# Optimization experiments

Measured on AMD Instinct MI355X. Metric: run time of the kernel, lower is better.

Reference implementation:

```python
import jax, jax.numpy as jnp
import numpy as np

N, E, D = 100000, 1600000, 128

def setup_inputs() -> dict:
    key = jax.random.key(0)
    ks = jax.random.split(key, 6)
    x = jax.random.normal(ks[0], (N, D), dtype=jnp.float32)
    edge_index = jax.random.randint(ks[1], (2, E), 0, N, dtype=jnp.int64)
    edge_weight = jax.random.uniform(ks[2], (E, 1), dtype=jnp.float32)
    s = 1.0 / np.sqrt(D)  # glorot-ish scale
    W1 = jax.random.normal(ks[3], (D, D), dtype=jnp.float32) * s
    b1 = jnp.zeros((D,), dtype=jnp.float32)
    W2 = jax.random.normal(ks[4], (D, D), dtype=jnp.float32) * s
    b2 = jnp.zeros((D,), dtype=jnp.float32)
    return {"x": x, "edge_index": edge_index, "edge_weight": edge_weight,
            "W1": W1, "b1": b1, "W2": W2, "b2": b2}

def reference(x, edge_index, edge_weight, W1, b1, W2, b2):
    # wh_1 = w1(x)  -- computed in the original forward but unused (dead code)
    wh_1 = x @ W1 + b1
    # gather source-node features: [E, D]
    x_j = x[edge_index[0]]
    # edge_weight reshaped to [E, 1], elementwise scale
    ew = edge_weight.reshape(-1, 1)
    # scatter-sum into destination nodes: [N, D]
    agg = jax.ops.segment_sum(x_j * ew, edge_index[1], num_segments=x.shape[0])
    wh_2 = agg @ W2 + b2
    return wh_2
```

## Files before the change

### kernel.cpp

```cpp
#include <hip/hip_runtime.h>

#define D 128
#define BSH 9
#define BNODES 512
#define NBUK 256
#define CAP_B 9216
#define CAP_S 11264
#define EPB 8192

typedef __attribute__((ext_vector_type(4))) float f32x4;
typedef __attribute__((ext_vector_type(8))) short bf16x8;

__device__ __forceinline__ unsigned short f2bf(float f) {
    unsigned u = __float_as_uint(f);
    u += 0x7FFFu + ((u >> 16) & 1u);
    return (unsigned short)(u >> 16);
}
__device__ __forceinline__ unsigned pack2(float a, float b) {
    return (unsigned)f2bf(a) | ((unsigned)f2bf(b) << 16);
}
__device__ __forceinline__ float bflo(unsigned v) { return __uint_as_float(v << 16); }
__device__ __forceinline__ float bfhi(unsigned v) { return __uint_as_float(v & 0xFFFF0000u); }

__global__ __launch_bounds__(256) void cvt_x_kernel(
        const float4* __restrict__ x4, uint2* __restrict__ xb, int n4,
        const float* __restrict__ W2, unsigned short* __restrict__ w2b,
        int* __restrict__ bcur) {
    int tid = blockIdx.x * blockDim.x + threadIdx.x;
    int stride = gridDim.x * blockDim.x;
    for (int i = tid; i < n4; i += stride) {
        float4 v = x4[i];
        xb[i] = make_uint2(pack2(v.x, v.y), pack2(v.z, v.w));
    }
    if (tid < D * D) {
        int j = tid >> 7, k = tid & 127;
        w2b[tid] = f2bf(W2[k * D + j]);
    }
    if (tid < NBUK) bcur[tid] = 0;
}

__global__ __launch_bounds__(256) void binify_kernel(
        const int* __restrict__ ei, const float* __restrict__ ew,
        int* __restrict__ bcur, uint2* __restrict__ brec, int E) {
    __shared__ int lh[NBUK];
    __shared__ int lbase[NBUK];
    int t = threadIdx.x;
    int base0 = blockIdx.x * EPB;
    lh[t] = 0;
    __syncthreads();

    #pragma unroll 4
    for (int u = 0; u < EPB / 512; ++u) {
        int e = base0 + u * 512 + t * 2;
        if (e + 1 < E) {
            int2 d2 = *(const int2*)(ei + E + e);
            atomicAdd(&lh[d2.x >> BSH], 1);
            atomicAdd(&lh[d2.y >> BSH], 1);
        } else if (e < E) {
            atomicAdd(&lh[ei[E + e] >> BSH], 1);
        }
    }
    __syncthreads();
    lbase[t] = (lh[t] > 0) ? atomicAdd(&bcur[t], lh[t]) : 0;
    lh[t] = 0;
    __syncthreads();

    #pragma unroll 4
    for (int u = 0; u < EPB / 512; ++u) {
        int e = base0 + u * 512 + t * 2;
        if (e + 1 < E) {
            int2 s2 = *(const int2*)(ei + e);
            int2 d2 = *(const int2*)(ei + E + e);
            float2 w2 = *(const float2*)(ew + e);
            int b0 = d2.x >> BSH;
            int p0 = lbase[b0] + atomicAdd(&lh[b0], 1);
            if (p0 < CAP_B)
                brec[(size_t)b0 * CAP_B + p0] = make_uint2(
                    ((unsigned)s2.x << BSH) | (unsigned)(d2.x & (BNODES - 1)),
                    __float_as_uint(w2.x));
            int b1 = d2.y >> BSH;
            int p1 = lbase[b1] + atomicAdd(&lh[b1], 1);
            if (p1 < CAP_B)
                brec[(size_t)b1 * CAP_B + p1] = make_uint2(
                    ((unsigned)s2.y << BSH) | (unsigned)(d2.y & (BNODES - 1)),
                    __float_as_uint(w2.y));
        } else if (e < E) {
            int b0 = ei[E + e] >> BSH;
            int p0 = lbase[b0] + atomicAdd(&lh[b0], 1);
            if (p0 < CAP_B)
                brec[(size_t)b0 * CAP_B + p0] = make_uint2(
                    ((unsigned)ei[e] << BSH) | (unsigned)(ei[E + e] & (BNODES - 1)),
                    __float_as_uint(ew[e]));
        }
    }
}

__global__ __launch_bounds__(256) void nodeify_kernel(
        const uint2* __restrict__ brec, const int* __restrict__ bcur,
        unsigned* __restrict__ srec, int2* __restrict__ offcnt, int N) {
    __shared__ int nh[BNODES];
    __shared__ int nb[BNODES];
    int b = blockIdx.x;
    int t = threadIdx.x;
    int cnt = bcur[b];
    if (cnt > CAP_B) cnt = CAP_B;
    const uint2* rec = brec + (size_t)b * CAP_B;

    nh[t] = 0; nh[t + 256] = 0;
    __syncthreads();
    for (int i = t; i < cnt; i += 256)
        atomicAdd(&nh[rec[i].x & (BNODES - 1)], 1);
    __syncthreads();

    int c0 = nh[2 * t], c1 = nh[2 * t + 1];
    int c0p = (c0 + 7) & ~7, c1p = (c1 + 7) & ~7;
    int run = c0p + c1p;
    nb[t] = run;
    __syncthreads();
    int val = run;
    for (int off = 1; off < 256; off <<= 1) {
        int other = (t >= off) ? nb[t - off] : 0;
        __syncthreads();
        val += other;
        nb[t] = val;
        __syncthreads();
    }
    int excl = val - run;
    __syncthreads();
    nb[2 * t] = excl;
    nb[2 * t + 1] = excl + c0p;

    int sbase = b * CAP_S;
    int node0 = b * BNODES;
    if (node0 + 2 * t < N)     offcnt[node0 + 2 * t]     = make_int2(sbase + excl,       c0p);
    if (node0 + 2 * t + 1 < N) offcnt[node0 + 2 * t + 1] = make_int2(sbase + excl + c0p, c1p);
    for (int p = c0; p < c0p; ++p) srec[(size_t)sbase + excl + p] = 0u;
    for (int p = c1; p < c1p; ++p) srec[(size_t)sbase + excl + c0p + p] = 0u;

    __syncthreads();
    nh[t] = 0; nh[t + 256] = 0;
    __syncthreads();

    for (int i = t; i < cnt; i += 256) {
        uint2 r = rec[i];
        int nl = r.x & (BNODES - 1);
        int rk = atomicAdd(&nh[nl], 1);
        unsigned src = r.x >> BSH;
        float w = __uint_as_float(r.y);
        int w15 = __float2int_rn(w * 32768.f);
        w15 = w15 < 0 ? 0 : (w15 > 32767 ? 32767 : w15);
        srec[(size_t)sbase + nb[nl] + rk] = (src << 15) | (unsigned)w15;
    }
}

__global__ __launch_bounds__(1024, 8) void gg_kernel(
        const unsigned* __restrict__ xb,
        const unsigned* __restrict__ srec,
        const int2* __restrict__ offcnt,
        const unsigned short* __restrict__ w2b,
        const float* __restrict__ b2,
        float* __restrict__ out, int N) {
    __shared__ unsigned At[16 * 66];
    int t = threadIdx.x, wave = t >> 6, lane = t & 63;
    int node0 = blockIdx.x * 16;
    int node = node0 + wave;

    int2 oc = offcnt[node];
    int beg = oc.x, total = oc.y;
    const char* xbase = (const char*)xb + lane * 4;
    float ax = 0.f, ay = 0.f;

    if (total <= 64) {
        unsigned rec = srec[beg + (lane < total ? lane : 0)];
        for (int r = 0; r + 8 <= total; r += 8) {
            unsigned q[8], v[8];
            #pragma unroll
            for (int u = 0; u < 8; ++u) q[u] = __shfl(rec, r + u);
            #pragma unroll
            for (int u = 0; u < 8; ++u)
                v[u] = *(const unsigned*)(xbase + ((q[u] & 0xFFFF8000u) >> 7));
            #pragma unroll
            for (int u = 0; u < 8; ++u) {
                float w = (float)(q[u] & 32767u);
                ax = fmaf(bflo(v[u]), w, ax);
                ay = fmaf(bfhi(v[u]), w, ay);
            }
        }
    } else {
        for (int j = beg; j < beg + total; ++j) {
            unsigned q0 = srec[j];
            unsigned v0 = *(const unsigned*)(xbase + ((q0 & 0xFFFF8000u) >> 7));
            float w0 = (float)(q0 & 32767u);
            ax = fmaf(bflo(v0), w0, ax);  ay = fmaf(bfhi(v0), w0, ay);
        }
    }
    At[wave * 66 + lane] = pack2(ax * (1.f / 32768.f), ay * (1.f / 32768.f));
    __syncthreads();

    if (wave < 8) {
        int r = lane & 15, g = lane >> 4;
        int col = wave * 16 + r;

        bf16x8 afr[4];
        #pragma unroll
        for (int kk = 0; kk < 4; ++kk)
            afr[kk] = *(const bf16x8*)((const char*)At + r * 264 + kk * 64 + g * 16);

        f32x4 acc = (f32x4){0.f, 0.f, 0.f, 0.f};
        #pragma unroll
        for (int kk = 0; kk < 4; ++kk) {
            bf16x8 bfr = *(const bf16x8*)(w2b + col * D + kk * 32 + g * 8);
            acc = __builtin_amdgcn_mfma_f32_16x16x32_bf16(afr[kk], bfr, acc, 0, 0, 0);
        }

        float bias = b2[col];
        float* o = out + (size_t)(node0 + g * 4) * D + col;
        o[0]     = acc[0] + bias;
        o[D]     = acc[1] + bias;
        o[2 * D] = acc[2] + bias;
        o[3 * D] = acc[3] + bias;
    }
}

extern "C" void kernel_launch(void* const* d_in, const int* in_sizes, int n_in,
                              void* d_out, int out_size, void* d_ws, size_t ws_size,
                              hipStream_t stream) {
    const float* x  = (const float*)d_in[0];
    const int*   ei = (const int*)d_in[1];
    const float* ew = (const float*)d_in[2];
    const float* W2 = (const float*)d_in[5];
    const float* b2 = (const float*)d_in[6];
    float* out = (float*)d_out;

    int N = in_sizes[0] / D;
    int E = in_sizes[2];

    int NB = (N + BNODES - 1) / BNODES;

    char* ws = (char*)d_ws;
    unsigned* xb   = (unsigned*)ws;
    uint2* brec    = (uint2*)(ws + (size_t)N * 256);
    unsigned* srec = (unsigned*)((char*)brec + (size_t)NB * CAP_B * 8);
    int2* offcnt   = (int2*)((char*)srec + (size_t)NB * CAP_S * 4);
    unsigned short* w2b = (unsigned short*)((char*)offcnt + (size_t)N * 8);
    int* bcur      = (int*)((char*)w2b + (size_t)D * D * 2);

    cvt_x_kernel<<<2048, 256, 0, stream>>>((const float4*)x, (uint2*)xb,
                                           N * D / 4, W2, w2b, bcur);

    binify_kernel<<<(E + EPB - 1) / EPB, 256, 0, stream>>>(ei, ew, bcur, brec, E);

    nodeify_kernel<<<NB, 256, 0, stream>>>(brec, bcur, srec, offcnt, N);

    gg_kernel<<<N / 16, 1024, 0, stream>>>(xb, srec, offcnt, w2b, b2, out, N);
}
```

Before: 138.3 us.

## Fuse x conversion with edge binning and double node tiles per GEMM block

Merges the x/W2 bf16 conversion kernel and the edge binning kernel into one launch that splits its blocks by role, so the two independent stages run concurrently. The bucket counter is now cleared with a memset, and the bucket record scratch is placed in the output buffer to shrink the workspace footprint. The gather+GEMM kernel now handles 32 nodes per block so all 16 waves issue MFMAs instead of half sitting idle. The risks are that reusing the output as scratch depends on its size covering the bucket records, and that N/32 truncation could skip tail nodes when N is not a multiple of 32.

```diff
diff --git a/kernel.cpp b/kernel.cpp
--- a/kernel.cpp
+++ b/kernel.cpp
@@ -22,75 +22,76 @@
 __device__ __forceinline__ float bflo(unsigned v) { return __uint_as_float(v << 16); }
 __device__ __forceinline__ float bfhi(unsigned v) { return __uint_as_float(v & 0xFFFF0000u); }
 
-__global__ __launch_bounds__(256) void cvt_x_kernel(
+__global__ __launch_bounds__(256) void cvtbin_kernel(
         const float4* __restrict__ x4, uint2* __restrict__ xb, int n4,
         const float* __restrict__ W2, unsigned short* __restrict__ w2b,
-        int* __restrict__ bcur) {
-    int tid = blockIdx.x * blockDim.x + threadIdx.x;
-    int stride = gridDim.x * blockDim.x;
-    for (int i = tid; i < n4; i += stride) {
-        float4 v = x4[i];
-        xb[i] = make_uint2(pack2(v.x, v.y), pack2(v.z, v.w));
-    }
-    if (tid < D * D) {
-        int j = tid >> 7, k = tid & 127;
-        w2b[tid] = f2bf(W2[k * D + j]);
-    }
-    if (tid < NBUK) bcur[tid] = 0;
-}
-
-__global__ __launch_bounds__(256) void binify_kernel(
         const int* __restrict__ ei, const float* __restrict__ ew,
-        int* __restrict__ bcur, uint2* __restrict__ brec, int E) {
+        int* __restrict__ bcur, uint2* __restrict__ brec, int E, int nbin) {
     __shared__ int lh[NBUK];
     __shared__ int lbase[NBUK];
     int t = threadIdx.x;
-    int base0 = blockIdx.x * EPB;
-    lh[t] = 0;
-    __syncthreads();
-
-    #pragma unroll 4
-    for (int u = 0; u < EPB / 512; ++u) {
-        int e = base0 + u * 512 + t * 2;
-        if (e + 1 < E) {
-            int2 d2 = *(const int2*)(ei + E + e);
-            atomicAdd(&lh[d2.x >> BSH], 1);
-            atomicAdd(&lh[d2.y >> BSH], 1);
-        } else if (e < E) {
-            atomicAdd(&lh[ei[E + e] >> BSH], 1);
-        }
-    }
-    __syncthreads();
-    lbase[t] = (lh[t] > 0) ? atomicAdd(&bcur[t], lh[t]) : 0;
-    lh[t] = 0;
-    __syncthreads();
-
-    #pragma unroll 4
-    for (int u = 0; u < EPB / 512; ++u) {
-        int e = base0 + u * 512 + t * 2;
-        if (e + 1 < E) {
-            int2 s2 = *(const int2*)(ei + e);
-            int2 d2 = *(const int2*)(ei + E + e);
-            float2 w2 = *(const float2*)(ew + e);
-            int b0 = d2.x >> BSH;
-            int p0 = lbase[b0] + atomicAdd(&lh[b0], 1);
-            if (p0 < CAP_B)
-                brec[(size_t)b0 * CAP_B + p0] = make_uint2(
-                    ((unsigned)s2.x << BSH) | (unsigned)(d2.x & (BNODES - 1)),
-                    __float_as_uint(w2.x));
-            int b1 = d2.y >> BSH;
-            int p1 = lbase[b1] + atomicAdd(&lh[b1], 1);
-            if (p1 < CAP_B)
-                brec[(size_t)b1 * CAP_B + p1] = make_uint2(
-                    ((unsigned)s2.y << BSH) | (unsigned)(d2.y & (BNODES - 1)),
-                    __float_as_uint(w2.y));
-        } else if (e < E) {
-            int b0 = ei[E + e] >> BSH;
-            int p0 = lbase[b0] + atomicAdd(&lh[b0], 1);
-            if (p0 < CAP_B)
-                brec[(size_t)b0 * CAP_B + p0] = make_uint2(
-                    ((unsigned)ei[e] << BSH) | (unsigned)(ei[E + e] & (BNODES - 1)),
-                    __float_as_uint(ew[e]));
+
+    if ((int)blockIdx.x < nbin) {
+        int base0 = blockIdx.x * EPB;
+        lh[t] = 0;
+        __syncthreads();
+
+        #pragma unroll 4
+        for (int u = 0; u < EPB / 512; ++u) {
+            int e = base0 + u * 512 + t * 2;
+            if (e + 1 < E) {
+                int2 d2 = *(const int2*)(ei + E + e);
+                atomicAdd(&lh[d2.x >> BSH], 1);
+                atomicAdd(&lh[d2.y >> BSH], 1);
+            } else if (e < E) {
+                atomicAdd(&lh[ei[E + e] >> BSH], 1);
+            }
+        }
+        __syncthreads();
+        lbase[t] = (lh[t] > 0) ? atomicAdd(&bcur[t], lh[t]) : 0;
+        lh[t] = 0;
+        __syncthreads();
+
+        #pragma unroll 4
+        for (int u = 0; u < EPB / 512; ++u) {
+            int e = base0 + u * 512 + t * 2;
+            if (e + 1 < E) {
+                int2 s2 = *(const int2*)(ei + e);
+                int2 d2 = *(const int2*)(ei + E + e);
+                float2 w2 = *(const float2*)(ew + e);
+                int b0 = d2.x >> BSH;
+                int p0 = lbase[b0] + atomicAdd(&lh[b0], 1);
+                if (p0 < CAP_B)
+                    brec[(size_t)b0 * CAP_B + p0] = make_uint2(
+                        ((unsigned)s2.x << BSH) | (unsigned)(d2.x & (BNODES - 1)),
+                        __float_as_uint(w2.x));
+                int b1 = d2.y >> BSH;
+                int p1 = lbase[b1] + atomicAdd(&lh[b1], 1);
+                if (p1 < CAP_B)
+                    brec[(size_t)b1 * CAP_B + p1] = make_uint2(
+                        ((unsigned)s2.y << BSH) | (unsigned)(d2.y & (BNODES - 1)),
+                        __float_as_uint(w2.y));
+            } else if (e < E) {
+                int b0 = ei[E + e] >> BSH;
+                int p0 = lbase[b0] + atomicAdd(&lh[b0], 1);
+                if (p0 < CAP_B)
+                    brec[(size_t)b0 * CAP_B + p0] = make_uint2(
+                        ((unsigned)ei[e] << BSH) | (unsigned)(ei[E + e] & (BNODES - 1)),
+                        __float_as_uint(ew[e]));
+            }
+        }
+    } else {
+        int bid = blockIdx.x - nbin;
+        int nblk = gridDim.x - nbin;
+        int tid = bid * 256 + t;
+        int stride = nblk * 256;
+        for (int i = tid; i < n4; i += stride) {
+            float4 v = x4[i];
+            xb[i] = make_uint2(pack2(v.x, v.y), pack2(v.z, v.w));
+        }
+        if (tid < D * D) {
+            int j = tid >> 7, k = tid & 127;
+            w2b[tid] = f2bf(W2[k * D + j]);
         }
     }
 }
@@ -153,23 +154,11 @@
     }
 }
 
-__global__ __launch_bounds__(1024, 8) void gg_kernel(
-        const unsigned* __restrict__ xb,
-        const unsigned* __restrict__ srec,
-        const int2* __restrict__ offcnt,
-        const unsigned short* __restrict__ w2b,
-        const float* __restrict__ b2,
-        float* __restrict__ out, int N) {
-    __shared__ unsigned At[16 * 66];
-    int t = threadIdx.x, wave = t >> 6, lane = t & 63;
-    int node0 = blockIdx.x * 16;
-    int node = node0 + wave;
-
-    int2 oc = offcnt[node];
+__device__ __forceinline__ unsigned gather_one(
+        const unsigned* __restrict__ srec, const char* xbase,
+        int2 oc, int lane) {
     int beg = oc.x, total = oc.y;
-    const char* xbase = (const char*)xb + lane * 4;
     float ax = 0.f, ay = 0.f;
-
     if (total <= 64) {
         unsigned rec = srec[beg + (lane < total ? lane : 0)];
         for (int r = 0; r + 8 <= total; r += 8) {
@@ -194,32 +183,49 @@
             ax = fmaf(bflo(v0), w0, ax);  ay = fmaf(bfhi(v0), w0, ay);
         }
     }
-    At[wave * 66 + lane] = pack2(ax * (1.f / 32768.f), ay * (1.f / 32768.f));
-    __syncthreads();
-
-    if (wave < 8) {
-        int r = lane & 15, g = lane >> 4;
-        int col = wave * 16 + r;
-
-        bf16x8 afr[4];
-        #pragma unroll
-        for (int kk = 0; kk < 4; ++kk)
-            afr[kk] = *(const bf16x8*)((const char*)At + r * 264 + kk * 64 + g * 16);
-
-        f32x4 acc = (f32x4){0.f, 0.f, 0.f, 0.f};
-        #pragma unroll
-        for (int kk = 0; kk < 4; ++kk) {
-            bf16x8 bfr = *(const bf16x8*)(w2b + col * D + kk * 32 + g * 8);
-            acc = __builtin_amdgcn_mfma_f32_16x16x32_bf16(afr[kk], bfr, acc, 0, 0, 0);
-        }
-
-        float bias = b2[col];
-        float* o = out + (size_t)(node0 + g * 4) * D + col;
-        o[0]     = acc[0] + bias;
-        o[D]     = acc[1] + bias;
-        o[2 * D] = acc[2] + bias;
-        o[3 * D] = acc[3] + bias;
-    }
+    return pack2(ax * (1.f / 32768.f), ay * (1.f / 32768.f));
+}
+
+__global__ __launch_bounds__(1024, 8) void gg_kernel(
+        const unsigned* __restrict__ xb,
+        const unsigned* __restrict__ srec,
+        const int2* __restrict__ offcnt,
+        const unsigned short* __restrict__ w2b,
+        const float* __restrict__ b2,
+        float* __restrict__ out, int N) {
+    __shared__ unsigned At[2][16 * 66];
+    int t = threadIdx.x, wave = t >> 6, lane = t & 63;
+    int node0 = blockIdx.x * 32;
+    const char* xbase = (const char*)xb + lane * 4;
+
+    int2 oc0 = offcnt[node0 + wave];
+    int2 oc1 = offcnt[node0 + 16 + wave];
+    At[0][wave * 66 + lane] = gather_one(srec, xbase, oc0, lane);
+    At[1][wave * 66 + lane] = gather_one(srec, xbase, oc1, lane);
+    __syncthreads();
+
+    int tt = wave >> 3, cg = wave & 7;
+    int r = lane & 15, g = lane >> 4;
+    int col = cg * 16 + r;
+
+    bf16x8 afr[4];
+    #pragma unroll
+    for (int kk = 0; kk < 4; ++kk)
+        afr[kk] = *(const bf16x8*)((const char*)At[tt] + r * 264 + kk * 64 + g * 16);
+
+    f32x4 acc = (f32x4){0.f, 0.f, 0.f, 0.f};
+    #pragma unroll
+    for (int kk = 0; kk < 4; ++kk) {
+        bf16x8 bfr = *(const bf16x8*)(w2b + col * D + kk * 32 + g * 8);
+        acc = __builtin_amdgcn_mfma_f32_16x16x32_bf16(afr[kk], bfr, acc, 0, 0, 0);
+    }
+
+    float bias = b2[col];
+    float* o = out + (size_t)(node0 + tt * 16 + g * 4) * D + col;
+    o[0]     = acc[0] + bias;
+    o[D]     = acc[1] + bias;
+    o[2 * D] = acc[2] + bias;
+    o[3 * D] = acc[3] + bias;
 }
 
 extern "C" void kernel_launch(void* const* d_in, const int* in_sizes, int n_in,
@@ -239,18 +245,20 @@
 
     char* ws = (char*)d_ws;
     unsigned* xb   = (unsigned*)ws;
-    uint2* brec    = (uint2*)(ws + (size_t)N * 256);
-    unsigned* srec = (unsigned*)((char*)brec + (size_t)NB * CAP_B * 8);
+    unsigned* srec = (unsigned*)(ws + (size_t)N * 256);
     int2* offcnt   = (int2*)((char*)srec + (size_t)NB * CAP_S * 4);
     unsigned short* w2b = (unsigned short*)((char*)offcnt + (size_t)N * 8);
     int* bcur      = (int*)((char*)w2b + (size_t)D * D * 2);
-
-    cvt_x_kernel<<<2048, 256, 0, stream>>>((const float4*)x, (uint2*)xb,
-                                           N * D / 4, W2, w2b, bcur);
-
-    binify_kernel<<<(E + EPB - 1) / EPB, 256, 0, stream>>>(ei, ew, bcur, brec, E);
+    uint2* brec    = (uint2*)d_out;
+
+    hipMemsetAsync(bcur, 0, NBUK * sizeof(int), stream);
+
+    int nbin = (E + EPB - 1) / EPB;
+    cvtbin_kernel<<<nbin + 1600, 256, 0, stream>>>(
+        (const float4*)x, (uint2*)xb, N * D / 4, W2, w2b,
+        ei, ew, bcur, brec, E, nbin);
 
     nodeify_kernel<<<NB, 256, 0, stream>>>(brec, bcur, srec, offcnt, N);
 
-    gg_kernel<<<N / 16, 1024, 0, stream>>>(xb, srec, offcnt, w2b, b2, out, N);
-}
+    gg_kernel<<<N / 32, 1024, 0, stream>>>(xb, srec, offcnt, w2b, b2, out, N);
+}
```

After: 141.9 us. +2.6%, slower.
